# Kernel tuning notes

Hardware: AMD Instinct MI355X
Metric: run time of the kernel (lower is better)

## Reference

```python
import jax, jax.numpy as jnp
import numpy as np
import math

B, S, D, H, L, DF = 16, 512, 512, 8, 6, 2048
DK = D // H
EPS = 1e-6


def _xavier(key, shape):
    # xavier_uniform over the last two dims (matches nn.init.xavier_uniform_)
    fan_in, fan_out = shape[-2], shape[-1]
    lim = math.sqrt(6.0 / (fan_in + fan_out))
    return jax.random.uniform(key, shape, jnp.float32, -lim, lim)


def setup_inputs() -> dict:
    key = jax.random.key(0)
    ks = jax.random.split(key, 12)
    return {
        "x": jax.random.normal(ks[0], (B, S, D), jnp.float32),
        "pe_table": jax.random.normal(ks[1], (S, D), jnp.float32),  # _4by8_pe weight
        "pe_q_w": _xavier(ks[2], (D, D)), "pe_q_b": jnp.zeros((D,), jnp.float32),
        "pe_k_w": _xavier(ks[3], (D, D)), "pe_k_b": jnp.zeros((D,), jnp.float32),
        "Wq": _xavier(ks[4], (L, D, D)), "bq": jnp.zeros((L, D), jnp.float32),
        "Wk": _xavier(ks[5], (L, D, D)), "bk": jnp.zeros((L, D), jnp.float32),
        "Wv": _xavier(ks[6], (L, D, D)), "bv": jnp.zeros((L, D), jnp.float32),
        "Wo": _xavier(ks[7], (L, D, D)), "bo": jnp.zeros((L, D), jnp.float32),
        "ln1_g": jnp.ones((L, D), jnp.float32), "ln1_b": jnp.zeros((L, D), jnp.float32),
        "W1": _xavier(ks[8], (L, D, DF)), "b1": jnp.zeros((L, DF), jnp.float32),
        "W2": _xavier(ks[9], (L, DF, D)), "b2": jnp.zeros((L, D), jnp.float32),
        "ln2_g": jnp.ones((L, D), jnp.float32), "ln2_b": jnp.zeros((L, D), jnp.float32),
    }


def _layernorm(y, g, b):
    m = jnp.mean(y, axis=-1, keepdims=True)
    v = jnp.var(y, axis=-1, keepdims=True)  # biased, as torch LayerNorm
    return (y - m) * jax.lax.rsqrt(v + EPS) * g + b


def reference(x, pe_table, pe_q_w, pe_q_b, pe_k_w, pe_k_b,
              Wq, bq, Wk, bk, Wv, bv, Wo, bo,
              ln1_g, ln1_b, W1, b1, W2, b2, ln2_g, ln2_b):
    scale = math.sqrt(2 * DK)
    h = x * math.sqrt(D)

    # scores_pe is identical for every batch element (pe_onehot = arange repeated)
    pq = (pe_table @ pe_q_w + pe_q_b).reshape(S, H, DK).transpose(1, 0, 2)  # [H,S,dk]
    pk = (pe_table @ pe_k_w + pe_k_b).reshape(S, H, DK).transpose(1, 0, 2)  # [H,S,dk]
    scores_pe = jnp.einsum('hqd,hkd->hqk', pq, pk) / scale  # [H,S,S]

    def step(h, p):
        wq, bq_, wk, bk_, wv, bv_, wo, bo_, g1, gb1, w1, fb1, w2, fb2, g2, gb2 = p
        q = (h @ wq + bq_).reshape(B, S, H, DK).transpose(0, 2, 1, 3)  # [B,H,S,dk]
        k = (h @ wk + bk_).reshape(B, S, H, DK).transpose(0, 2, 1, 3)
        v = (h @ wv + bv_).reshape(B, S, H, DK).transpose(0, 2, 1, 3)
        scores = jnp.einsum('bhqd,bhkd->bhqk', q, k) / scale + scores_pe  # [B,H,S,S]
        attn = jax.nn.softmax(scores, axis=-1)
        o = jnp.einsum('bhqk,bhkd->bhqd', attn, v).transpose(0, 2, 1, 3).reshape(B, S, D)
        o = o @ wo + bo_
        h1 = _layernorm(o + h, g1, gb1)
        f = jax.nn.gelu(h1 @ w1 + fb1, approximate=False) @ w2 + fb2
        h2 = _layernorm(f + h1, g2, gb2)
        return h2, None

    params = (Wq, bq, Wk, bk, Wv, bv, Wo, bo, ln1_g, ln1_b, W1, b1, W2, b2, ln2_g, ln2_b)
    h, _ = jax.lax.scan(step, h, params)
    pe_out = jnp.broadcast_to(pe_table, (B, S, D))
    return h, pe_out
```

## Files before the change

kernel.cpp:

```cpp
#include <hip/hip_runtime.h>
#include <hip/hip_bf16.h>

typedef __hip_bfloat16 bf16;
typedef short bf16x8 __attribute__((ext_vector_type(8)));
typedef float f32x4 __attribute__((ext_vector_type(4)));

#define DEV static __device__ __forceinline__

DEV f32x4 fzero4(){ f32x4 z; z[0]=0.f; z[1]=0.f; z[2]=0.f; z[3]=0.f; return z; }

DEV float bf2f(bf16 v){
  unsigned int u = ((unsigned int)*(unsigned short*)&v) << 16;
  return *(float*)&u;
}
DEV float bf2s(short s){
  unsigned int u = ((unsigned int)(unsigned short)s) << 16;
  return *(float*)&u;
}

DEV void gl2lds16(const bf16* g, bf16* l){
  __builtin_amdgcn_global_load_lds(
    (const __attribute__((address_space(1))) void*)g,
    (__attribute__((address_space(3))) void*)l, 16, 0, 0);
}

enum { EP_F32=0, EP_BF16=1, EP_GELU=2, EP_HILO=3, EP_QKV=4 };

template<int EPI, int NMT>
__global__ __launch_bounds__(256) void gemm_bt(
    const bf16* A0, const bf16* A1, const bf16* A2,
    const bf16* B0, const bf16* B1, const bf16* B2,
    int npass, int lda, int ldb, int M, int N, int K,
    const float* __restrict__ bs0, const float* __restrict__ bs1, const float* __restrict__ bs2,
    float alpha, void* o0, void* o1, void* o2,
    int nn, int mchunk, int azs, int bzs, int ozs)
{
  constexpr int BM = NMT*32;
  __shared__ __align__(16) bf16 As[2][BM*32];
  __shared__ __align__(16) bf16 Bs[2][128*32];
  const int t = threadIdx.x;
  const int lane = t & 63;
  const int w = t >> 6;
  const int wr = w >> 1, wc = w & 1;
  const int bid = blockIdx.x;
  const int xcd = bid & 7;
  const int idx = bid >> 3;
  const int qm = idx / nn;
  const int mb = xcd*mchunk + qm;
  const int nb = idx - qm*nn;
  const int m0 = mb*BM, n0 = nb*128;
  const int l15 = lane & 15, l4 = lane >> 4;
  const int grow = (lane >> 2);
  const int gcol = (lane & 3) * 8;
  const int z = blockIdx.z;
  if (azs){ A0 += (size_t)z*azs; if(A1) A1 += (size_t)z*azs; if(A2) A2 += (size_t)z*azs; }
  if (bzs){ B0 += (size_t)z*bzs; if(B1) B1 += (size_t)z*bzs; if(B2) B2 += (size_t)z*bzs; }

  auto Aof = [&](int p){ return (p==0)?A0:((p==1)?A1:A2); };
  auto Bof = [&](int p){ return (p==0)?B0:((p==1)?B1:B2); };

  auto stageAB = [&](int cb, const bf16* Ag, const bf16* Bg, int k0){
    if constexpr (NMT==4){
      #pragma unroll
      for (int q=0;q<2;q++){
        int row = w*32 + q*16 + grow;
        gl2lds16(Ag + (size_t)(m0+row)*lda + k0 + gcol, As[cb] + (w*32+q*16)*32);
        gl2lds16(Bg + (size_t)(n0+row)*ldb + k0 + gcol, Bs[cb] + (w*32+q*16)*32);
      }
    } else {
      int rA = w*16 + grow;
      gl2lds16(Ag + (size_t)(m0+rA)*lda + k0 + gcol, As[cb] + w*16*32);
      #pragma unroll
      for (int sb=0;sb<2;sb++){
        int rB = (2*w+sb)*16 + grow;
        gl2lds16(Bg + (size_t)(n0+rB)*ldb + k0 + gcol, Bs[cb] + (2*w+sb)*16*32);
      }
    }
  };

  f32x4 acc[NMT][4];
  #pragma unroll
  for (int i=0;i<NMT;i++)
    #pragma unroll
    for (int j=0;j<4;j++) acc[i][j] = fzero4();

  int cur = 0;
  stageAB(0, A0, B0, 0);
  for (int p=0;p<npass;p++){
    for (int k0=0;k0<K;k0+=32){
      __syncthreads();
      int kn = k0 + 32;
      if (kn < K)            stageAB(cur^1, Aof(p), Bof(p), kn);
      else if (p+1 < npass)  stageAB(cur^1, Aof(p+1), Bof(p+1), 0);
      bf16x8 af[NMT], bfv[4];
      #pragma unroll
      for (int mt=0;mt<NMT;mt++) af[mt] = *(const bf16x8*)(As[cur] + (wr*(NMT*16)+mt*16+l15)*32 + 8*l4);
      #pragma unroll
      for (int nt=0;nt<4;nt++) bfv[nt] = *(const bf16x8*)(Bs[cur] + (wc*64+nt*16+l15)*32 + 8*l4);
      #pragma unroll
      for (int mt=0;mt<NMT;mt++)
        #pragma unroll
        for (int nt=0;nt<4;nt++)
          acc[mt][nt] = __builtin_amdgcn_mfma_f32_16x16x32_bf16(af[mt], bfv[nt], acc[mt][nt], 0, 0, 0);
      cur ^= 1;
    }
  }

  #pragma unroll
  for (int mt=0;mt<NMT;mt++){
    #pragma unroll
    for (int nt=0;nt<4;nt++){
      const int crow = m0 + wr*(NMT*16) + mt*16 + l4*4;
      const int ccol = n0 + wc*64 + nt*16 + l15;
      #pragma unroll
      for (int j=0;j<4;j++){
        float v = acc[mt][nt][j];
        int r = crow + j;
        if (EPI==EP_F32){
          float b = bs0 ? bs0[ccol] : 0.f;
          ((float*)o0)[(size_t)r*N + ccol] = alpha*v + b;
        } else if (EPI==EP_BF16){
          float b = bs0 ? bs0[ccol] : 0.f;
          ((bf16*)o0 + (size_t)z*ozs)[(size_t)r*N + ccol] = __float2bfloat16(alpha*v + b);
        } else if (EPI==EP_GELU){
          float xx = v + bs0[ccol];
          float g = 0.5f*xx*(1.f + erff(xx*0.70710678118654752f));
          ((bf16*)o0)[(size_t)r*N + ccol] = __float2bfloat16(g);
        } else if (EPI==EP_HILO){
          float xx = (v + bs0[ccol]) * alpha;
          bf16 hi = __float2bfloat16(xx);
          ((bf16*)o0)[(size_t)r*N + ccol] = hi;
          ((bf16*)o1)[(size_t)r*N + ccol] = __float2bfloat16(xx - bf2f(hi));
        } else {
          int n = ccol;
          if (n < 512){
            ((bf16*)o0)[(size_t)r*512 + n] = __float2bfloat16((v + bs0[n]) * alpha);
          } else if (n < 1024){
            ((bf16*)o1)[(size_t)r*512 + (n-512)] = __float2bfloat16(v + bs1[n-512]);
          } else {
            int d = n - 1024;
            int bb = r >> 9, s = r & 511;
            int hh = d >> 6, dd = d & 63;
            ((bf16*)o2)[(size_t)(((bb*8)+hh)*64 + dd)*512 + s] = __float2bfloat16(v + bs2[d]);
          }
        }
      }
    }
  }
}

template<int SPLIT>
__global__ __launch_bounds__(256) void attn_mfma(
  const bf16* __restrict__ Q, const bf16* __restrict__ Qlo,
  const bf16* __restrict__ Kh, const bf16* __restrict__ Klo,
  const bf16* __restrict__ VT, const bf16* __restrict__ SPE,
  bf16* __restrict__ O)
{
  __shared__ __align__(16) bf16 K_lds[64*64];
  __shared__ __align__(16) bf16 V_lds[64*64];
  __shared__ __align__(16) bf16 Klo_lds[SPLIT ? 64*64 : 8];
  __shared__ __align__(16) bf16 P_lds[4][16*64];
  const int t = threadIdx.x;
  const int lane = t & 63, w = t >> 6;
  const int l15 = lane & 15, l4 = lane >> 4;
  const int bid = blockIdx.x;
  const int h = bid & 7;
  const int s2 = bid >> 3;
  const int b = s2 >> 3, qblk = s2 & 7;
  const int q0 = qblk*64 + w*16;
  const int xorv = (l15 & 7) << 3;

  bf16x8 qf[2], qflo[2];
  #pragma unroll
  for (int kst=0;kst<2;kst++){
    qf[kst] = *(const bf16x8*)(Q + (size_t)(b*512 + q0 + l15)*512 + h*64 + kst*32 + 8*l4);
    if (SPLIT) qflo[kst] = *(const bf16x8*)(Qlo + (size_t)(b*512 + q0 + l15)*512 + h*64 + kst*32 + 8*l4);
  }
  f32x4 accO[4];
  #pragma unroll
  for (int dt=0;dt<4;dt++) accO[dt] = fzero4();
  float mrow[4], lrow[4];
  #pragma unroll
  for (int j=0;j<4;j++){ mrow[j] = -1e30f; lrow[j] = 0.f; }

  const bf16* spe_h = SPE + (size_t)h*262144;
  const bf16* vbase = VT + (size_t)((b*8)+h)*32768;

  for (int n0=0;n0<512;n0+=64){
    #pragma unroll
    for (int st=0;st<2;st++){
      int rl = w*16 + st*8 + (lane>>3);
      int jj = (lane&7) ^ (rl&7);
      gl2lds16(Kh + (size_t)(b*512 + n0 + rl)*512 + h*64 + jj*8, K_lds + (w*16+st*8)*64);
      if (SPLIT)
        gl2lds16(Klo + (size_t)(b*512 + n0 + rl)*512 + h*64 + jj*8, Klo_lds + (w*16+st*8)*64);
      gl2lds16(vbase + (size_t)rl*512 + n0 + jj*8, V_lds + (w*16+st*8)*64);
    }
    __syncthreads();

    f32x4 sc[4];
    #pragma unroll
    for (int c=0;c<4;c++) sc[c] = fzero4();
    #pragma unroll
    for (int c=0;c<4;c++){
      const int rr = c*16 + l15;
      #pragma unroll
      for (int kst=0;kst<2;kst++){
        bf16x8 kf = *(const bf16x8*)(K_lds + rr*64 + ((kst*32 + 8*l4) ^ xorv));
        sc[c] = __builtin_amdgcn_mfma_f32_16x16x32_bf16(qf[kst], kf, sc[c], 0,0,0);
        if (SPLIT){
          sc[c] = __builtin_amdgcn_mfma_f32_16x16x32_bf16(qflo[kst], kf, sc[c], 0,0,0);
          bf16x8 kfl = *(const bf16x8*)(Klo_lds + rr*64 + ((kst*32 + 8*l4) ^ xorv));
          sc[c] = __builtin_amdgcn_mfma_f32_16x16x32_bf16(qf[kst], kfl, sc[c], 0,0,0);
        }
      }
    }
    float sv[4][4];
    #pragma unroll
    for (int c=0;c<4;c++)
      #pragma unroll
      for (int j=0;j<4;j++){
        int qr = q0 + l4*4 + j;
        sv[c][j] = sc[c][j] + bf2f(spe_h[(size_t)qr*512 + n0 + c*16 + l15]);
      }
    float mx[4];
    float dm = -1e30f;
    #pragma unroll
    for (int j=0;j<4;j++){
      mx[j] = fmaxf(fmaxf(sv[0][j],sv[1][j]), fmaxf(sv[2][j],sv[3][j]));
      dm = fmaxf(dm, mx[j] - mrow[j]);
    }
    if (__any(dm > 12.f)){
      #pragma unroll
      for (int j=0;j<4;j++){
        float m2 = mx[j];
        m2 = fmaxf(m2, __shfl_xor(m2,1));
        m2 = fmaxf(m2, __shfl_xor(m2,2));
        m2 = fmaxf(m2, __shfl_xor(m2,4));
        m2 = fmaxf(m2, __shfl_xor(m2,8));
        float mn = fmaxf(mrow[j], m2);
        float fac = exp2f(mrow[j] - mn);
        mrow[j] = mn;
        lrow[j] *= fac;
        #pragma unroll
        for (int dt=0;dt<4;dt++) accO[dt][j] *= fac;
      }
    }
    #pragma unroll
    for (int j=0;j<4;j++){
      int row = l4*4 + j;
      float ts = 0.f;
      #pragma unroll
      for (int c=0;c<4;c++){
        float pv = exp2f(sv[c][j] - mrow[j]);
        ts += pv;
        P_lds[w][row*64 + ((c*16 + l15) ^ ((row&7)<<3))] = __float2bfloat16(pv);
      }
      ts += __shfl_xor(ts,1); ts += __shfl_xor(ts,2);
      ts += __shfl_xor(ts,4); ts += __shfl_xor(ts,8);
      lrow[j] += ts;
    }
    #pragma unroll
    for (int kv=0;kv<2;kv++){
      bf16x8 pf = *(const bf16x8*)(P_lds[w] + l15*64 + ((kv*32 + 8*l4) ^ xorv));
      #pragma unroll
      for (int dt=0;dt<4;dt++){
        const int d = dt*16 + l15;
        bf16x8 vf = *(const bf16x8*)(V_lds + d*64 + ((kv*32 + 8*l4) ^ xorv));
        accO[dt] = __builtin_amdgcn_mfma_f32_16x16x32_bf16(pf, vf, accO[dt], 0,0,0);
      }
    }
    __syncthreads();
  }
  #pragma unroll
  for (int dt=0;dt<4;dt++)
    #pragma unroll
    for (int j=0;j<4;j++){
      float v = accO[dt][j] / lrow[j];
      int r = q0 + l4*4 + j;
      O[(size_t)(b*512+r)*512 + h*64 + dt*16 + l15] = __float2bfloat16(v);
    }
}

__global__ __launch_bounds__(256) void ln_kernel(
  const bf16* __restrict__ tmp, const float* __restrict__ resid,
  const float* __restrict__ g, const float* __restrict__ bta,
  float* __restrict__ outf, bf16* __restrict__ outb)
{
  const int row = blockIdx.x*4 + (threadIdx.x>>6);
  const int lane = threadIdx.x & 63;
  const size_t base = (size_t)row*512 + lane*8;
  bf16x8 a = *(const bf16x8*)(tmp+base);
  float4 r0 = *(const float4*)(resid+base), r1 = *(const float4*)(resid+base+4);
  float x[8];
  x[0]=bf2s(a[0])+r0.x; x[1]=bf2s(a[1])+r0.y;
  x[2]=bf2s(a[2])+r0.z; x[3]=bf2s(a[3])+r0.w;
  x[4]=bf2s(a[4])+r1.x; x[5]=bf2s(a[5])+r1.y;
  x[6]=bf2s(a[6])+r1.z; x[7]=bf2s(a[7])+r1.w;
  float s=0.f, sq=0.f;
  #pragma unroll
  for (int i=0;i<8;i++){ s += x[i]; sq += x[i]*x[i]; }
  #pragma unroll
  for (int d=1; d<64; d<<=1){ s += __shfl_xor(s,d); sq += __shfl_xor(sq,d); }
  float mean = s*(1.f/512.f);
  float var = sq*(1.f/512.f) - mean*mean;
  float rr = rsqrtf(var + 1e-6f);
  #pragma unroll
  for (int i=0;i<8;i++){
    int d = lane*8 + i;
    float y = (x[i]-mean)*rr*g[d] + bta[d];
    outf[base+i] = y;
    outb[base+i] = __float2bfloat16(y);
  }
}

template<bool LO>
__global__ __launch_bounds__(256) void tcast(
  const float* __restrict__ src, int srcStride,
  bf16* __restrict__ dst, int dstStride, bf16* __restrict__ dlo,
  int R, int C)
{
  __shared__ float tile[32][33];
  const int z = blockIdx.z;
  src += (size_t)z*srcStride;
  dst += (size_t)z*dstStride;
  const int tx = threadIdx.x & 31, ty = threadIdx.x >> 5;
  const int r0 = blockIdx.y*32, c0 = blockIdx.x*32;
  #pragma unroll
  for (int p=0;p<4;p++)
    tile[ty+8*p][tx] = src[(size_t)(r0+ty+8*p)*C + c0+tx];
  __syncthreads();
  #pragma unroll
  for (int p=0;p<4;p++){
    float v = tile[tx][ty+8*p];
    bf16 hi = __float2bfloat16(v);
    dst[(size_t)(c0+ty+8*p)*R + r0+tx] = hi;
    if (LO) dlo[(size_t)(c0+ty+8*p)*R + r0+tx] = __float2bfloat16(v - bf2f(hi));
  }
}

__global__ void castbf(const float* __restrict__ in, bf16* __restrict__ out, int n){
  int i = blockIdx.x*blockDim.x + threadIdx.x;
  if (i < n) out[i] = __float2bfloat16(in[i]);
}

__global__ void init_h(const float* __restrict__ x, float* __restrict__ hf,
                       bf16* __restrict__ hb, bf16* __restrict__ hlo, int n){
  int i = blockIdx.x*blockDim.x + threadIdx.x;
  if (i < n){
    float v = x[i]*22.627416997969522f;
    hf[i] = v;
    bf16 hi = __float2bfloat16(v);
    hb[i] = hi;
    hlo[i] = __float2bfloat16(v - bf2f(hi));
  }
}

__global__ void write_out(const float* __restrict__ hf, const float* __restrict__ pe,
                          float* __restrict__ out, int n1){
  int i = blockIdx.x*blockDim.x + threadIdx.x;
  if (i < n1){
    out[i] = hf[i];
    out[n1 + i] = pe[i & 262143];
  }
}

extern "C" void kernel_launch(void* const* d_in, const int* in_sizes, int n_in,
                              void* d_out, int out_size, void* d_ws, size_t ws_size,
                              hipStream_t stream)
{
  const float* x    = (const float*)d_in[0];
  const float* pe   = (const float*)d_in[1];
  const float* peqw = (const float*)d_in[2];
  const float* peqb = (const float*)d_in[3];
  const float* pekw = (const float*)d_in[4];
  const float* pekb = (const float*)d_in[5];
  const float* Wq   = (const float*)d_in[6];
  const float* bq   = (const float*)d_in[7];
  const float* Wk   = (const float*)d_in[8];
  const float* bk   = (const float*)d_in[9];
  const float* Wv   = (const float*)d_in[10];
  const float* bv   = (const float*)d_in[11];
  const float* Wo   = (const float*)d_in[12];
  const float* bo   = (const float*)d_in[13];
  const float* g1   = (const float*)d_in[14];
  const float* bb1  = (const float*)d_in[15];
  const float* W1   = (const float*)d_in[16];
  const float* fb1  = (const float*)d_in[17];
  const float* W2   = (const float*)d_in[18];
  const float* fb2  = (const float*)d_in[19];
  const float* g2   = (const float*)d_in[20];
  const float* bb2  = (const float*)d_in[21];

  char* wp = (char*)d_ws;
  auto carve = [&](size_t bytes)->void*{ void* r = (void*)wp; wp += (bytes + 255) & ~(size_t)255; return r; };
  float* hf   = (float*)carve(16777216);
  float* h1f  = (float*)carve(16777216);
  char*  regB = (char*)carve(16777216);
  bf16*  tmpb = (bf16*)regB;
  bf16*  qlo  = (bf16*)regB;
  bf16*  klo  = (bf16*)(regB + 8388608);
  bf16* hb    = (bf16*)carve(8388608);
  bf16* hlo   = (bf16*)carve(8388608);
  bf16* h1b   = (bf16*)carve(8388608);
  char* regA  = (char*)carve(33554432);
  bf16* gbuf  = (bf16*)regA;
  bf16* qb    = (bf16*)regA;
  bf16* kbuf  = (bf16*)(regA + 8388608);
  bf16* vT    = (bf16*)(regA + 16777216);
  bf16* obuf  = (bf16*)(regA + 25165824);
  bf16* WqkvT = (bf16*)carve(9437184);
  bf16* WoT   = (bf16*)carve(3145728);
  bf16* W1T   = (bf16*)carve(12582912);
  bf16* W2T   = (bf16*)carve(12582912);
  bf16* Wq0h  = (bf16*)carve(524288);
  bf16* Wq0l  = (bf16*)carve(524288);
  bf16* Wk0h  = (bf16*)carve(524288);
  bf16* Wk0l  = (bf16*)carve(524288);
  bf16* peb   = (bf16*)carve(524288);
  bf16* pqwT  = (bf16*)carve(524288);
  bf16* pkwT  = (bf16*)carve(524288);
  bf16* pqb   = (bf16*)carve(524288);
  bf16* pkb   = (bf16*)carve(524288);
  bf16* spe   = (bf16*)carve(4194304);

  dim3 B256(256);
  const float QSCALE = 0.08838834764831845f * 1.4426950408889634f;

  tcast<false><<<dim3(16,16,6),B256,0,stream>>>(Wq, 262144, WqkvT,          786432, nullptr, 512, 512);
  tcast<false><<<dim3(16,16,6),B256,0,stream>>>(Wk, 262144, WqkvT + 262144, 786432, nullptr, 512, 512);
  tcast<false><<<dim3(16,16,6),B256,0,stream>>>(Wv, 262144, WqkvT + 524288, 786432, nullptr, 512, 512);
  tcast<false><<<dim3(16,16,6),B256,0,stream>>>(Wo, 262144, WoT, 262144, nullptr, 512, 512);
  tcast<false><<<dim3(64,16,6),B256,0,stream>>>(W1, 1048576, W1T, 1048576, nullptr, 512, 2048);
  tcast<false><<<dim3(16,64,6),B256,0,stream>>>(W2, 1048576, W2T, 1048576, nullptr, 2048, 512);
  tcast<false><<<dim3(16,16,1),B256,0,stream>>>(peqw, 262144, pqwT, 262144, nullptr, 512, 512);
  tcast<false><<<dim3(16,16,1),B256,0,stream>>>(pekw, 262144, pkwT, 262144, nullptr, 512, 512);
  tcast<true ><<<dim3(16,16,1),B256,0,stream>>>(Wq, 262144, Wq0h, 262144, Wq0l, 512, 512);
  tcast<true ><<<dim3(16,16,1),B256,0,stream>>>(Wk, 262144, Wk0h, 262144, Wk0l, 512, 512);
  castbf<<<1024,B256,0,stream>>>(pe, peb, 262144);
  init_h<<<16384,B256,0,stream>>>(x, hf, hb, hlo, 4194304);

  gemm_bt<EP_BF16,2><<<dim3(32),B256,0,stream>>>(peb,nullptr,nullptr, pqwT,nullptr,nullptr, 1, 512,512, 512,512,512, peqb,nullptr,nullptr, 1.f, pqb,nullptr,nullptr, 4,1, 0,0,0);
  gemm_bt<EP_BF16,2><<<dim3(32),B256,0,stream>>>(peb,nullptr,nullptr, pkwT,nullptr,nullptr, 1, 512,512, 512,512,512, pekb,nullptr,nullptr, 1.f, pkb,nullptr,nullptr, 4,1, 0,0,0);
  gemm_bt<EP_BF16,2><<<dim3(32,1,8),B256,0,stream>>>(pqb,nullptr,nullptr, pkb,nullptr,nullptr, 1, 512,512, 512,512,64, nullptr,nullptr,nullptr, QSCALE, spe,nullptr,nullptr, 4,1, 64,64,262144);

  for (int l=0;l<6;l++){
    const bf16* WQKV = WqkvT + l*786432;
    const float* bql = bq + l*512;
    const float* bkl = bk + l*512;
    const float* bvl = bv + l*512;
    gemm_bt<EP_QKV,4><<<dim3(768),B256,0,stream>>>(hb,nullptr,nullptr, WQKV,nullptr,nullptr, 1, 512,512, 8192,1536,512, bql,bkl,bvl, QSCALE, qb, kbuf, vT, 12,8, 0,0,0);
    if (l==0){
      gemm_bt<EP_HILO,2><<<dim3(512),B256,0,stream>>>(hb,hb,hlo, Wq0h,Wq0l,Wq0h, 3, 512,512, 8192,512,512, bql,nullptr,nullptr, QSCALE, qb, qlo, nullptr, 4,16, 0,0,0);
      gemm_bt<EP_HILO,2><<<dim3(512),B256,0,stream>>>(hb,hb,hlo, Wk0h,Wk0l,Wk0h, 3, 512,512, 8192,512,512, bkl,nullptr,nullptr, 1.f, kbuf, klo, nullptr, 4,16, 0,0,0);
      attn_mfma<1><<<dim3(1024),B256,0,stream>>>(qb,qlo,kbuf,klo,vT,spe,obuf);
    } else {
      attn_mfma<0><<<dim3(1024),B256,0,stream>>>(qb,qb,kbuf,kbuf,vT,spe,obuf);
    }
    gemm_bt<EP_BF16,2><<<dim3(512),B256,0,stream>>>(obuf,nullptr,nullptr, WoT+l*262144,nullptr,nullptr, 1, 512,512, 8192,512,512, bo+l*512,nullptr,nullptr, 1.f, tmpb,nullptr,nullptr, 4,16, 0,0,0);
    ln_kernel<<<2048,B256,0,stream>>>(tmpb, hf, g1+l*512, bb1+l*512, h1f, h1b);
    gemm_bt<EP_GELU,4><<<dim3(1024),B256,0,stream>>>(h1b,nullptr,nullptr, W1T+l*1048576,nullptr,nullptr, 1, 512,512, 8192,2048,512, fb1+l*2048,nullptr,nullptr, 1.f, gbuf,nullptr,nullptr, 16,8, 0,0,0);
    gemm_bt<EP_BF16,2><<<dim3(512),B256,0,stream>>>(gbuf,nullptr,nullptr, W2T+l*1048576,nullptr,nullptr, 1, 2048,2048, 8192,512,2048, fb2+l*512,nullptr,nullptr, 1.f, tmpb,nullptr,nullptr, 4,16, 0,0,0);
    ln_kernel<<<2048,B256,0,stream>>>(tmpb, h1f, g2+l*512, bb2+l*512, hf, hb);
  }
  write_out<<<16384,B256,0,stream>>>(hf, pe, (float*)d_out, 4194304);
}
```

Baseline: 1.279 ms.

## Drop lazy softmax rescale, unfold scale into attention, write final LN to output

The attention kernel no longer folds the 1/sqrt(2dk)*log2e scale into Q. It multiplies the raw scores by the inverse scale inside the loop, uses __expf, and always rescales the running max and accumulators instead of only when the max grows past a threshold. The last layer's LayerNorm now writes directly into the output buffer, so the final kernel only writes the broadcast PE table and no longer copies h. This saves one full-size copy but adds an unconditional max reduction, rescale and per-score multiply to every attention tile.

After: 1.284 ms. Within noise of the previous version (+0.3%).

```diff
diff --git a/kernel.cpp b/kernel.cpp
--- a/kernel.cpp
+++ b/kernel.cpp
@@ -168,6 +168,7 @@
   const int s2 = bid >> 3;
   const int b = s2 >> 3, qblk = s2 & 7;
   const int q0 = qblk*64 + w*16;
+  const float inv_scale = 0.08838834764831845f;
   const int xorv = (l15 & 7) << 3;
 
   bf16x8 qf[2], qflo[2];
@@ -221,30 +222,19 @@
       #pragma unroll
       for (int j=0;j<4;j++){
         int qr = q0 + l4*4 + j;
-        sv[c][j] = sc[c][j] + bf2f(spe_h[(size_t)qr*512 + n0 + c*16 + l15]);
-      }
-    float mx[4];
-    float dm = -1e30f;
+        sv[c][j] = sc[c][j]*inv_scale + bf2f(spe_h[(size_t)qr*512 + n0 + c*16 + l15]);
+      }
+    float fac[4];
     #pragma unroll
     for (int j=0;j<4;j++){
-      mx[j] = fmaxf(fmaxf(sv[0][j],sv[1][j]), fmaxf(sv[2][j],sv[3][j]));
-      dm = fmaxf(dm, mx[j] - mrow[j]);
-    }
-    if (__any(dm > 12.f)){
-      #pragma unroll
-      for (int j=0;j<4;j++){
-        float m2 = mx[j];
-        m2 = fmaxf(m2, __shfl_xor(m2,1));
-        m2 = fmaxf(m2, __shfl_xor(m2,2));
-        m2 = fmaxf(m2, __shfl_xor(m2,4));
-        m2 = fmaxf(m2, __shfl_xor(m2,8));
-        float mn = fmaxf(mrow[j], m2);
-        float fac = exp2f(mrow[j] - mn);
-        mrow[j] = mn;
-        lrow[j] *= fac;
-        #pragma unroll
-        for (int dt=0;dt<4;dt++) accO[dt][j] *= fac;
-      }
+      float m2 = fmaxf(fmaxf(sv[0][j],sv[1][j]), fmaxf(sv[2][j],sv[3][j]));
+      m2 = fmaxf(m2, __shfl_xor(m2,1));
+      m2 = fmaxf(m2, __shfl_xor(m2,2));
+      m2 = fmaxf(m2, __shfl_xor(m2,4));
+      m2 = fmaxf(m2, __shfl_xor(m2,8));
+      float mn = fmaxf(mrow[j], m2);
+      fac[j] = __expf(mrow[j] - mn);
+      mrow[j] = mn;
     }
     #pragma unroll
     for (int j=0;j<4;j++){
@@ -252,13 +242,15 @@
       float ts = 0.f;
       #pragma unroll
       for (int c=0;c<4;c++){
-        float pv = exp2f(sv[c][j] - mrow[j]);
+        float pv = __expf(sv[c][j] - mrow[j]);
         ts += pv;
         P_lds[w][row*64 + ((c*16 + l15) ^ ((row&7)<<3))] = __float2bfloat16(pv);
       }
       ts += __shfl_xor(ts,1); ts += __shfl_xor(ts,2);
       ts += __shfl_xor(ts,4); ts += __shfl_xor(ts,8);
-      lrow[j] += ts;
+      lrow[j] = lrow[j]*fac[j] + ts;
+      #pragma unroll
+      for (int dt=0;dt<4;dt++) accO[dt][j] *= fac[j];
     }
     #pragma unroll
     for (int kv=0;kv<2;kv++){
@@ -356,13 +348,9 @@
   }
 }
 
-__global__ void write_out(const float* __restrict__ hf, const float* __restrict__ pe,
-                          float* __restrict__ out, int n1){
+__global__ void pe_out(const float* __restrict__ pe, float* __restrict__ out, int n1){
   int i = blockIdx.x*blockDim.x + threadIdx.x;
-  if (i < n1){
-    out[i] = hf[i];
-    out[n1 + i] = pe[i & 262143];
-  }
+  if (i < n1) out[n1 + i] = pe[i & 262143];
 }
 
 extern "C" void kernel_launch(void* const* d_in, const int* in_sizes, int n_in,
@@ -425,7 +413,7 @@
   bf16* spe   = (bf16*)carve(4194304);
 
   dim3 B256(256);
-  const float QSCALE = 0.08838834764831845f * 1.4426950408889634f;
+  const float INV_SCALE = 0.08838834764831845f;
 
   tcast<false><<<dim3(16,16,6),B256,0,stream>>>(Wq, 262144, WqkvT,          786432, nullptr, 512, 512);
   tcast<false><<<dim3(16,16,6),B256,0,stream>>>(Wk, 262144, WqkvT + 262144, 786432, nullptr, 512, 512);
@@ -442,16 +430,16 @@
 
   gemm_bt<EP_BF16,2><<<dim3(32),B256,0,stream>>>(peb,nullptr,nullptr, pqwT,nullptr,nullptr, 1, 512,512, 512,512,512, peqb,nullptr,nullptr, 1.f, pqb,nullptr,nullptr, 4,1, 0,0,0);
   gemm_bt<EP_BF16,2><<<dim3(32),B256,0,stream>>>(peb,nullptr,nullptr, pkwT,nullptr,nullptr, 1, 512,512, 512,512,512, pekb,nullptr,nullptr, 1.f, pkb,nullptr,nullptr, 4,1, 0,0,0);
-  gemm_bt<EP_BF16,2><<<dim3(32,1,8),B256,0,stream>>>(pqb,nullptr,nullptr, pkb,nullptr,nullptr, 1, 512,512, 512,512,64, nullptr,nullptr,nullptr, QSCALE, spe,nullptr,nullptr, 4,1, 64,64,262144);
+  gemm_bt<EP_BF16,2><<<dim3(32,1,8),B256,0,stream>>>(pqb,nullptr,nullptr, pkb,nullptr,nullptr, 1, 512,512, 512,512,64, nullptr,nullptr,nullptr, INV_SCALE, spe,nullptr,nullptr, 4,1, 64,64,262144);
 
   for (int l=0;l<6;l++){
     const bf16* WQKV = WqkvT + l*786432;
     const float* bql = bq + l*512;
     const float* bkl = bk + l*512;
     const float* bvl = bv + l*512;
-    gemm_bt<EP_QKV,4><<<dim3(768),B256,0,stream>>>(hb,nullptr,nullptr, WQKV,nullptr,nullptr, 1, 512,512, 8192,1536,512, bql,bkl,bvl, QSCALE, qb, kbuf, vT, 12,8, 0,0,0);
+    gemm_bt<EP_QKV,4><<<dim3(768),B256,0,stream>>>(hb,nullptr,nullptr, WQKV,nullptr,nullptr, 1, 512,512, 8192,1536,512, bql,bkl,bvl, 1.f, qb, kbuf, vT, 12,8, 0,0,0);
     if (l==0){
-      gemm_bt<EP_HILO,2><<<dim3(512),B256,0,stream>>>(hb,hb,hlo, Wq0h,Wq0l,Wq0h, 3, 512,512, 8192,512,512, bql,nullptr,nullptr, QSCALE, qb, qlo, nullptr, 4,16, 0,0,0);
+      gemm_bt<EP_HILO,2><<<dim3(512),B256,0,stream>>>(hb,hb,hlo, Wq0h,Wq0l,Wq0h, 3, 512,512, 8192,512,512, bql,nullptr,nullptr, 1.f, qb, qlo, nullptr, 4,16, 0,0,0);
       gemm_bt<EP_HILO,2><<<dim3(512),B256,0,stream>>>(hb,hb,hlo, Wk0h,Wk0l,Wk0h, 3, 512,512, 8192,512,512, bkl,nullptr,nullptr, 1.f, kbuf, klo, nullptr, 4,16, 0,0,0);
       attn_mfma<1><<<dim3(1024),B256,0,stream>>>(qb,qlo,kbuf,klo,vT,spe,obuf);
     } else {
@@ -461,7 +449,8 @@
     ln_kernel<<<2048,B256,0,stream>>>(tmpb, hf, g1+l*512, bb1+l*512, h1f, h1b);
     gemm_bt<EP_GELU,4><<<dim3(1024),B256,0,stream>>>(h1b,nullptr,nullptr, W1T+l*1048576,nullptr,nullptr, 1, 512,512, 8192,2048,512, fb1+l*2048,nullptr,nullptr, 1.f, gbuf,nullptr,nullptr, 16,8, 0,0,0);
     gemm_bt<EP_BF16,2><<<dim3(512),B256,0,stream>>>(gbuf,nullptr,nullptr, W2T+l*1048576,nullptr,nullptr, 1, 2048,2048, 8192,512,2048, fb2+l*512,nullptr,nullptr, 1.f, tmpb,nullptr,nullptr, 4,16, 0,0,0);
-    ln_kernel<<<2048,B256,0,stream>>>(tmpb, h1f, g2+l*512, bb2+l*512, hf, hb);
-  }
-  write_out<<<16384,B256,0,stream>>>(hf, pe, (float*)d_out, 4194304);
-}
+    ln_kernel<<<2048,B256,0,stream>>>(tmpb, h1f, g2+l*512, bb2+l*512,
+                                      (l==5) ? (float*)d_out : hf, hb);
+  }
+  pe_out<<<16384,B256,0,stream>>>(pe, (float*)d_out, 4194304);
+}
```
